# Kernel optimization log

Hardware: AMD Instinct MI355X
Metric: run time of the kernel (lower is better)

The kernel has to match this reference:

```python
import jax, jax.numpy as jnp
import numpy as np

N, D = 6144, 128
NUM_CLASSES, NUM_BATCHES = 20, 5
MIN_T, MAX_T = 0.1, 1.0
TEMP_BATCH = 0.5  # fixed per-batch-key temperature set in __init__
EPS = 1e-8        # F.cosine_similarity eps


def _class_weights(labels, n):
    c = jnp.bincount(labels, length=n).astype(jnp.float32)
    w = 1.0 / c
    return w / w.sum()


def setup_inputs() -> dict:
    key = jax.random.key(0)
    k1, k2, k3 = jax.random.split(key, 3)
    x = jax.random.normal(k1, (N, D), dtype=jnp.float32)
    targets = jax.random.randint(k2, (N,), 0, NUM_CLASSES)
    batch0 = jax.random.randint(k3, (N,), 0, NUM_BATCHES)
    return {
        "input": x,
        "temperature": jnp.float32(0.25),
        "weight_target": _class_weights(targets, NUM_CLASSES),
        "weight_batch0": _class_weights(batch0, NUM_BATCHES),
        "targets": targets,
        "batch0": batch0,
    }


def _snn_losses(S, pos_mask, neg_mask):
    # S: [N,N] exp-similarities; masks include/exclude self consistently with torch code
    diag = jnp.diagonal(S)
    pos_sum = jnp.einsum('ij,ij->i', S, pos_mask.astype(S.dtype)) - diag  # self is in pos_mask
    neg_sum = jnp.einsum('ij,ij->i', S, neg_mask.astype(S.dtype))
    cnt_pos = pos_mask.sum(axis=1)  # includes self
    cnt_neg = neg_mask.sum(axis=1)
    valid = (cnt_pos >= 2) & (cnt_neg >= 1)
    pos_safe = jnp.where(valid, pos_sum, 1.0)
    neg_safe = jnp.where(valid, neg_sum, 1.0)
    loss_i = -jnp.log(pos_safe / (pos_safe + neg_safe))
    return loss_i, valid


def _weighted_class_sum(loss_i, valid, labels, weights, num_segments):
    lsum = jax.ops.segment_sum(jnp.where(valid, loss_i, 0.0), labels, num_segments=num_segments)
    cnt = jax.ops.segment_sum(valid.astype(jnp.float32), labels, num_segments=num_segments)
    mean = lsum / jnp.maximum(cnt, 1.0)
    return jnp.sum(jnp.where(cnt > 0, mean * weights, 0.0))


def reference(input, temperature, weight_target, weight_batch0, targets, batch0):
    t = jnp.clip(temperature, MIN_T, MAX_T)
    norms = jnp.maximum(jnp.linalg.norm(input, axis=1, keepdims=True), EPS)
    xn = input / norms
    sim = xn @ xn.T  # [N, N] cosine similarity

    same_t = targets[:, None] == targets[None, :]

    # ----- target (cell-type) SNN loss -----
    S_t = jnp.exp(sim / t)
    loss_i, valid = _snn_losses(S_t, same_t, ~same_t)
    loss_target = _weighted_class_sum(loss_i, valid, targets, weight_target, NUM_CLASSES)

    # ----- batch-effect loss (one batch key), reciprocal of -log -----
    S_b = jnp.exp(sim / TEMP_BATCH)
    same_b = batch0[:, None] == batch0[None, :]
    pos_mask = same_t & same_b
    neg_mask = same_t & (~same_b)
    loss_bi, valid_b = _snn_losses(S_b, pos_mask, neg_mask)
    loss_bi = jnp.where(valid_b, 1.0 / jnp.where(valid_b, loss_bi, 1.0), 0.0)
    loss_batch = _weighted_class_sum(loss_bi, valid_b, batch0, weight_batch0, NUM_BATCHES)
    # single batch key -> mean over batch keys is just loss_batch

    return 0.9 * loss_target + 0.1 * loss_batch
```

## Files before the change

kernel.cpp:

```cpp
#include <hip/hip_runtime.h>
#include <hip/hip_bf16.h>
#include <math.h>

#define NN 6144
#define DD 128
#define NCLS 20
#define NBATCH 5
#define NB 48
#define NPAIR (NB * (NB + 1) / 2)

typedef float f32x4 __attribute__((ext_vector_type(4)));
typedef short bf16x8 __attribute__((ext_vector_type(8)));

#define SOFF (NN * DD / 2)
#define AOFF (SOFF + 4 * NN)
#define COFF (AOFF + 50)

__global__ __launch_bounds__(256) void k_prep(const float* __restrict__ x,
                                              float* __restrict__ ws) {
    const int t = threadIdx.x;
    if (blockIdx.x < 24) {
        float4 z = {0.f, 0.f, 0.f, 0.f};
        *(float4*)(ws + SOFF + blockIdx.x * 1024 + t * 4) = z;
    } else if (blockIdx.x == 24) {
        if (t < 51) ws[AOFF + t] = 0.0f;
    }
    const int lane = t & 63;
    const int row = blockIdx.x * 4 + (t >> 6);
    float2 v = *(const float2*)(x + row * DD + 2 * lane);
    float s = v.x * v.x + v.y * v.y;
#pragma unroll
    for (int m = 1; m < 64; m <<= 1) s += __shfl_xor(s, m, 64);
    float rinv = 1.0f / fmaxf(sqrtf(s), 1e-8f);
    __hip_bfloat16 h0 = __float2bfloat16(v.x * rinv);
    __hip_bfloat16 h1 = __float2bfloat16(v.y * rinv);
    ushort2 u;
    u.x = *(ushort*)&h0;
    u.y = *(ushort*)&h1;
    ushort* xnb = (ushort*)ws;
    *(ushort2*)(xnb + row * DD + 2 * lane) = u;
}

#define RED16(v)                                                      \
    {                                                                 \
        float s0 = up3 ? v[0] : v[2], k0 = up3 ? v[2] : v[0];         \
        float s1 = up3 ? v[1] : v[3], k1 = up3 ? v[3] : v[1];         \
        v[0] = k0 + __shfl_xor(s0, 8, 64);                            \
        v[1] = k1 + __shfl_xor(s1, 8, 64);                            \
        float s2 = up2 ? v[0] : v[1], k2 = up2 ? v[1] : v[0];         \
        v[0] = k2 + __shfl_xor(s2, 4, 64);                            \
        v[0] += __shfl_xor(v[0], 2, 64);                              \
        v[0] += __shfl_xor(v[0], 1, 64);                              \
    }

#define RED4(v)                                                       \
    {                                                                 \
        float s0 = q1 ? v[0] : v[2], k0 = q1 ? v[2] : v[0];           \
        float s1 = q1 ? v[1] : v[3], k1 = q1 ? v[3] : v[1];           \
        v[0] = k0 + __shfl_xor(s0, 32, 64);                           \
        v[1] = k1 + __shfl_xor(s1, 32, 64);                           \
        float s2 = q0 ? v[0] : v[1], k2 = q0 ? v[1] : v[0];           \
        v[0] = k2 + __shfl_xor(s2, 16, 64);                           \
    }

__global__ __launch_bounds__(256) void k_main(const float* __restrict__ temp,
                                              const int* __restrict__ tg,
                                              const int* __restrict__ bt,
                                              float* __restrict__ ws) {
    __shared__ ushort tA[128][72];
    __shared__ ushort tB[128][72];
    __shared__ int tgA[128], btA[128], tgB[128], btB[128];
    __shared__ float sRow[2][4][128];
    __shared__ float sCol[2][4][128];

    const ushort* xnb = (const ushort*)ws;
    float* PT = ws + SOFF;
    float* TT = PT + NN;
    float* PB = PT + 2 * NN;
    float* TB = PT + 3 * NN;

    int bi = 0, rem = blockIdx.x;
    while (rem >= NB - bi) { rem -= NB - bi; ++bi; }
    const int bj = bi + rem;
    const int I = bi * 128, J = bj * 128;
    const bool isDiag = (bi == bj);

    const int t = threadIdx.x;
    const int w = t >> 6;
    const int lane = t & 63;
    const int tx16 = lane & 15;
    const int quad = lane >> 4;
    const int rowBase = (w >> 1) * 64;
    const int colBase = (w & 1) * 64;

    const float tc = fminf(fmaxf(temp[0], 0.1f), 1.0f);
    const float c1 = 1.4426950408889634f / tc;
    const float c2 = 2.8853900817779268f;

    if (t < 128) { tgA[t] = tg[I + t]; btA[t] = bt[I + t]; }
    else { int u2 = t - 128; tgB[u2] = tg[J + u2]; btB[u2] = bt[J + u2]; }
    {
        float* zr = &sRow[0][0][0];
        float* zc = &sCol[0][0][0];
#pragma unroll
        for (int i = 0; i < 4; ++i) { zr[t + 256 * i] = 0.f; zc[t + 256 * i] = 0.f; }
    }

    f32x4 acc[4][4];
#pragma unroll
    for (int mt = 0; mt < 4; ++mt)
#pragma unroll
        for (int nt = 0; nt < 4; ++nt) acc[mt][nt] = (f32x4){0.f, 0.f, 0.f, 0.f};

    for (int kc = 0; kc < 2; ++kc) {
        if (kc) __syncthreads();
        {
            const int r0 = t >> 3, ch = t & 7;
            const ushort* gA = xnb + (I + r0) * DD + kc * 64 + ch * 8;
            const ushort* gB = xnb + (J + r0) * DD + kc * 64 + ch * 8;
#pragma unroll
            for (int it = 0; it < 4; ++it) {
                *(float4*)&tA[r0 + 32 * it][ch * 8] = *(const float4*)(gA + 32 * it * DD);
                *(float4*)&tB[r0 + 32 * it][ch * 8] = *(const float4*)(gB + 32 * it * DD);
            }
        }
        __syncthreads();
#pragma unroll
        for (int ks = 0; ks < 2; ++ks) {
            bf16x8 a[4], b[4];
            const int ko = ks * 32 + quad * 8;
#pragma unroll
            for (int mt = 0; mt < 4; ++mt)
                a[mt] = *(const bf16x8*)&tA[rowBase + 16 * mt + tx16][ko];
#pragma unroll
            for (int nt = 0; nt < 4; ++nt)
                b[nt] = *(const bf16x8*)&tB[colBase + 16 * nt + tx16][ko];
#pragma unroll
            for (int mt = 0; mt < 4; ++mt)
#pragma unroll
                for (int nt = 0; nt < 4; ++nt)
                    acc[mt][nt] = __builtin_amdgcn_mfma_f32_16x16x32_bf16(
                        a[mt], b[nt], acc[mt][nt], 0, 0, 0);
        }
    }

    float cPT[4] = {0}, cTT[4] = {0}, cPB[4] = {0}, cTB[4] = {0};
    int tjv[4], bjv[4];
#pragma unroll
    for (int nt = 0; nt < 4; ++nt) {
        int jl = colBase + 16 * nt + tx16;
        tjv[nt] = tgB[jl];
        bjv[nt] = btB[jl];
    }
    const bool up3 = (tx16 >> 3) & 1;
    const bool up2 = (tx16 >> 2) & 1;
    const int pOwn = tx16 >> 2;

#pragma unroll
    for (int mt = 0; mt < 4; ++mt) {
        float rPT[4] = {0}, rTT[4] = {0}, rPB[4] = {0}, rTB[4] = {0};
        int til[4], bil[4];
#pragma unroll
        for (int p = 0; p < 4; ++p) {
            int il = rowBase + 16 * mt + 4 * quad + p;
            til[p] = tgA[il];
            bil[p] = btA[il];
        }
#pragma unroll
        for (int nt = 0; nt < 4; ++nt) {
            const int jl = colBase + 16 * nt + tx16;
#pragma unroll
            for (int p = 0; p < 4; ++p) {
                const int il = rowBase + 16 * mt + 4 * quad + p;
                float s = acc[mt][nt][p];
                float et = __builtin_amdgcn_exp2f(c1 * s);
                float eb = __builtin_amdgcn_exp2f(c2 * s);
                bool nd = !isDiag || (il != jl);
                bool st = (til[p] == tjv[nt]) && nd;
                bool sb = (bil[p] == bjv[nt]);
                rTT[p] += nd ? et : 0.f;
                rPT[p] += st ? et : 0.f;
                rTB[p] += st ? eb : 0.f;
                rPB[p] += (st && sb) ? eb : 0.f;
                if (!isDiag) {
                    cTT[nt] += et;
                    cPT[nt] += st ? et : 0.f;
                    cTB[nt] += st ? eb : 0.f;
                    cPB[nt] += (st && sb) ? eb : 0.f;
                }
            }
        }
        RED16(rPT);
        RED16(rTT);
        RED16(rPB);
        RED16(rTB);
        if ((tx16 & 3) == 0) {
            int il = rowBase + 16 * mt + 4 * quad + pOwn;
            sRow[w & 1][0][il] = rPT[0];
            sRow[w & 1][1][il] = rTT[0];
            sRow[w & 1][2][il] = rPB[0];
            sRow[w & 1][3][il] = rTB[0];
        }
    }
    if (!isDiag) {
        const bool q1 = (quad >> 1) & 1;
        const bool q0 = quad & 1;
        RED4(cPT);
        RED4(cTT);
        RED4(cPB);
        RED4(cTB);
        int cl = colBase + 16 * quad + tx16;
        sCol[w >> 1][0][cl] = cPT[0];
        sCol[w >> 1][1][cl] = cTT[0];
        sCol[w >> 1][2][cl] = cPB[0];
        sCol[w >> 1][3][cl] = cTB[0];
    }

    __syncthreads();
    if (t < 128) {
        int gi = I + t;
        atomicAdd(&PT[gi], sRow[0][0][t] + sRow[1][0][t]);
        atomicAdd(&TT[gi], sRow[0][1][t] + sRow[1][1][t]);
        atomicAdd(&PB[gi], sRow[0][2][t] + sRow[1][2][t]);
        atomicAdd(&TB[gi], sRow[0][3][t] + sRow[1][3][t]);
    } else if (!isDiag) {
        int u2 = t - 128;
        int gj = J + u2;
        atomicAdd(&PT[gj], sCol[0][0][u2] + sCol[1][0][u2]);
        atomicAdd(&TT[gj], sCol[0][1][u2] + sCol[1][1][u2]);
        atomicAdd(&PB[gj], sCol[0][2][u2] + sCol[1][2][u2]);
        atomicAdd(&TB[gj], sCol[0][3][u2] + sCol[1][3][u2]);
    }
}

__global__ __launch_bounds__(256) void k_fin(const int* __restrict__ tg,
                                             const int* __restrict__ bt,
                                             const float* __restrict__ wt,
                                             const float* __restrict__ wb,
                                             float* __restrict__ ws,
                                             float* __restrict__ out) {
    __shared__ int hh[NCLS + NCLS * NBATCH];
    __shared__ float ph[4][52];
    __shared__ int lastFlag;
    const int t = threadIdx.x;
    const int wv = t >> 6;
    if (t < NCLS + NCLS * NBATCH) hh[t] = 0;
    if (t < 52 * 4) ((float*)ph)[t] = 0.0f;
    __syncthreads();
    for (int i = t; i < NN; i += 256) {
        int c = tg[i], b = bt[i];
        atomicAdd(&hh[c], 1);
        atomicAdd(&hh[NCLS + c * NBATCH + b], 1);
    }
    __syncthreads();
    const float* PT = ws + SOFF;
    const float* TT = PT + NN;
    const float* PB = PT + 2 * NN;
    const float* TB = PT + 3 * NN;
    {
        const int i = blockIdx.x * 256 + t;
        float pt = PT[i], tt = TT[i], pb = PB[i], tb = TB[i];
        int ti = tg[i], bi = bt[i];
        int cp = hh[ti];
        int cpb = hh[NCLS + ti * NBATCH + bi];
        if (cp >= 2 && (NN - cp) >= 1) {
            float loss = logf(tt) - logf(pt);
            atomicAdd(&ph[wv][ti], loss);
            atomicAdd(&ph[wv][20 + ti], 1.0f);
        }
        if (cpb >= 2 && (cp - cpb) >= 1) {
            float lb = logf(tb) - logf(pb);
            atomicAdd(&ph[wv][40 + bi], 1.0f / lb);
            atomicAdd(&ph[wv][45 + bi], 1.0f);
        }
    }
    __syncthreads();
    if (t < 50) {
        float s = ph[0][t] + ph[1][t] + ph[2][t] + ph[3][t];
        atomicAdd(&ws[AOFF + t], s);
    }
    __syncthreads();
    if (t == 0) {
        __threadfence();
        int old = atomicAdd((int*)(ws + COFF), 1);
        lastFlag = (old == 23) ? 1 : 0;
    }
    __syncthreads();
    if (lastFlag) {
        __threadfence();
        if (t < 64) {
            const float* acc = ws + AOFF;
            float term = 0.0f;
            if (t < NCLS) {
                float cnt = acc[NCLS + t];
                if (cnt > 0.f) term = 0.9f * (acc[t] / cnt) * wt[t];
            } else if (t >= 32 && t < 32 + NBATCH) {
                int b = t - 32;
                float cnt = acc[2 * NCLS + NBATCH + b];
                if (cnt > 0.f) term = 0.1f * (acc[2 * NCLS + b] / cnt) * wb[b];
            }
#pragma unroll
            for (int m = 1; m < 64; m <<= 1) term += __shfl_xor(term, m, 64);
            if (t == 0) out[0] = term;
        }
    }
}

extern "C" void kernel_launch(void* const* d_in, const int* in_sizes, int n_in,
                              void* d_out, int out_size, void* d_ws, size_t ws_size,
                              hipStream_t stream) {
    const float* x    = (const float*)d_in[0];
    const float* temp = (const float*)d_in[1];
    const float* wt   = (const float*)d_in[2];
    const float* wb   = (const float*)d_in[3];
    const int*   tg   = (const int*)d_in[4];
    const int*   bt   = (const int*)d_in[5];
    float* out = (float*)d_out;
    float* ws = (float*)d_ws;

    k_prep<<<NN / 4, 256, 0, stream>>>(x, ws);
    k_main<<<NPAIR, 256, 0, stream>>>(temp, tg, bt, ws);
    k_fin<<<24, 256, 0, stream>>>(tg, bt, wt, wb, ws, out);
}
```

Measured before the change: 102.6 us.

## Fuse finalize into main kernel via last-block reduction and alias shared memory

```diff
diff --git a/kernel.cpp b/kernel.cpp
--- a/kernel.cpp
+++ b/kernel.cpp
@@ -13,8 +13,7 @@
 typedef short bf16x8 __attribute__((ext_vector_type(8)));
 
 #define SOFF (NN * DD / 2)
-#define AOFF (SOFF + 4 * NN)
-#define COFF (AOFF + 50)
+#define COFF (SOFF + 4 * NN)
 
 __global__ __launch_bounds__(256) void k_prep(const float* __restrict__ x,
                                               float* __restrict__ ws) {
@@ -23,7 +22,7 @@
         float4 z = {0.f, 0.f, 0.f, 0.f};
         *(float4*)(ws + SOFF + blockIdx.x * 1024 + t * 4) = z;
     } else if (blockIdx.x == 24) {
-        if (t < 51) ws[AOFF + t] = 0.0f;
+        if (t == 0) ((int*)ws)[COFF] = 0;
     }
     const int lane = t & 63;
     const int row = blockIdx.x * 4 + (t >> 6);
@@ -66,12 +65,18 @@
 __global__ __launch_bounds__(256) void k_main(const float* __restrict__ temp,
                                               const int* __restrict__ tg,
                                               const int* __restrict__ bt,
-                                              float* __restrict__ ws) {
-    __shared__ ushort tA[128][72];
-    __shared__ ushort tB[128][72];
+                                              const float* __restrict__ wt,
+                                              const float* __restrict__ wb,
+                                              float* __restrict__ ws,
+                                              float* __restrict__ out) {
+    __shared__ __align__(16) char smem[34816];
     __shared__ int tgA[128], btA[128], tgB[128], btB[128];
-    __shared__ float sRow[2][4][128];
-    __shared__ float sCol[2][4][128];
+    __shared__ int lastFlag;
+
+    ushort (*tA)[68] = (ushort(*)[68])smem;
+    ushort (*tB)[68] = (ushort(*)[68])(smem + 17408);
+    float* sRowF = (float*)smem;
+    float* sColF = (float*)(smem + 4096);
 
     const ushort* xnb = (const ushort*)ws;
     float* PT = ws + SOFF;
@@ -99,12 +104,6 @@
 
     if (t < 128) { tgA[t] = tg[I + t]; btA[t] = bt[I + t]; }
     else { int u2 = t - 128; tgB[u2] = tg[J + u2]; btB[u2] = bt[J + u2]; }
-    {
-        float* zr = &sRow[0][0][0];
-        float* zc = &sCol[0][0][0];
-#pragma unroll
-        for (int i = 0; i < 4; ++i) { zr[t + 256 * i] = 0.f; zc[t + 256 * i] = 0.f; }
-    }
 
     f32x4 acc[4][4];
 #pragma unroll
@@ -144,6 +143,8 @@
         }
     }
 
+    __syncthreads();
+
     float cPT[4] = {0}, cTT[4] = {0}, cPB[4] = {0}, cTB[4] = {0};
     int tjv[4], bjv[4];
 #pragma unroll
@@ -166,27 +167,46 @@
             til[p] = tgA[il];
             bil[p] = btA[il];
         }
-#pragma unroll
-        for (int nt = 0; nt < 4; ++nt) {
-            const int jl = colBase + 16 * nt + tx16;
-#pragma unroll
-            for (int p = 0; p < 4; ++p) {
-                const int il = rowBase + 16 * mt + 4 * quad + p;
-                float s = acc[mt][nt][p];
-                float et = __builtin_amdgcn_exp2f(c1 * s);
-                float eb = __builtin_amdgcn_exp2f(c2 * s);
-                bool nd = !isDiag || (il != jl);
-                bool st = (til[p] == tjv[nt]) && nd;
-                bool sb = (bil[p] == bjv[nt]);
-                rTT[p] += nd ? et : 0.f;
-                rPT[p] += st ? et : 0.f;
-                rTB[p] += st ? eb : 0.f;
-                rPB[p] += (st && sb) ? eb : 0.f;
-                if (!isDiag) {
+        if (isDiag) {
+#pragma unroll
+            for (int nt = 0; nt < 4; ++nt) {
+                const int jl = colBase + 16 * nt + tx16;
+#pragma unroll
+                for (int p = 0; p < 4; ++p) {
+                    const int il = rowBase + 16 * mt + 4 * quad + p;
+                    float s = acc[mt][nt][p];
+                    float et = __builtin_amdgcn_exp2f(c1 * s);
+                    float eb = __builtin_amdgcn_exp2f(c2 * s);
+                    bool nd = (il != jl);
+                    bool st = (til[p] == tjv[nt]) && nd;
+                    bool sb = (bil[p] == bjv[nt]);
+                    rTT[p] += nd ? et : 0.f;
+                    rPT[p] += st ? et : 0.f;
+                    rTB[p] += st ? eb : 0.f;
+                    rPB[p] += (st && sb) ? eb : 0.f;
+                }
+            }
+        } else {
+#pragma unroll
+            for (int nt = 0; nt < 4; ++nt) {
+#pragma unroll
+                for (int p = 0; p < 4; ++p) {
+                    float s = acc[mt][nt][p];
+                    float et = __builtin_amdgcn_exp2f(c1 * s);
+                    float eb = __builtin_amdgcn_exp2f(c2 * s);
+                    bool st = (til[p] == tjv[nt]);
+                    bool sb = (bil[p] == bjv[nt]);
+                    float etp = st ? et : 0.f;
+                    float ebp = st ? eb : 0.f;
+                    float ebb = (st && sb) ? eb : 0.f;
+                    rTT[p] += et;
+                    rPT[p] += etp;
+                    rTB[p] += ebp;
+                    rPB[p] += ebb;
                     cTT[nt] += et;
-                    cPT[nt] += st ? et : 0.f;
-                    cTB[nt] += st ? eb : 0.f;
-                    cPB[nt] += (st && sb) ? eb : 0.f;
+                    cPT[nt] += etp;
+                    cTB[nt] += ebp;
+                    cPB[nt] += ebb;
                 }
             }
         }
@@ -196,10 +216,11 @@
         RED16(rTB);
         if ((tx16 & 3) == 0) {
             int il = rowBase + 16 * mt + 4 * quad + pOwn;
-            sRow[w & 1][0][il] = rPT[0];
-            sRow[w & 1][1][il] = rTT[0];
-            sRow[w & 1][2][il] = rPB[0];
-            sRow[w & 1][3][il] = rTB[0];
+            int rep = (w & 1) * 512;
+            sRowF[rep + 0 * 128 + il] = rPT[0];
+            sRowF[rep + 1 * 128 + il] = rTT[0];
+            sRowF[rep + 2 * 128 + il] = rPB[0];
+            sRowF[rep + 3 * 128 + il] = rTB[0];
         }
     }
     if (!isDiag) {
@@ -210,99 +231,87 @@
         RED4(cPB);
         RED4(cTB);
         int cl = colBase + 16 * quad + tx16;
-        sCol[w >> 1][0][cl] = cPT[0];
-        sCol[w >> 1][1][cl] = cTT[0];
-        sCol[w >> 1][2][cl] = cPB[0];
-        sCol[w >> 1][3][cl] = cTB[0];
+        int rep = (w >> 1) * 512;
+        sColF[rep + 0 * 128 + cl] = cPT[0];
+        sColF[rep + 1 * 128 + cl] = cTT[0];
+        sColF[rep + 2 * 128 + cl] = cPB[0];
+        sColF[rep + 3 * 128 + cl] = cTB[0];
     }
 
     __syncthreads();
     if (t < 128) {
         int gi = I + t;
-        atomicAdd(&PT[gi], sRow[0][0][t] + sRow[1][0][t]);
-        atomicAdd(&TT[gi], sRow[0][1][t] + sRow[1][1][t]);
-        atomicAdd(&PB[gi], sRow[0][2][t] + sRow[1][2][t]);
-        atomicAdd(&TB[gi], sRow[0][3][t] + sRow[1][3][t]);
+        atomicAdd(&PT[gi], sRowF[0 * 128 + t] + sRowF[512 + 0 * 128 + t]);
+        atomicAdd(&TT[gi], sRowF[1 * 128 + t] + sRowF[512 + 1 * 128 + t]);
+        atomicAdd(&PB[gi], sRowF[2 * 128 + t] + sRowF[512 + 2 * 128 + t]);
+        atomicAdd(&TB[gi], sRowF[3 * 128 + t] + sRowF[512 + 3 * 128 + t]);
     } else if (!isDiag) {
         int u2 = t - 128;
         int gj = J + u2;
-        atomicAdd(&PT[gj], sCol[0][0][u2] + sCol[1][0][u2]);
-        atomicAdd(&TT[gj], sCol[0][1][u2] + sCol[1][1][u2]);
-        atomicAdd(&PB[gj], sCol[0][2][u2] + sCol[1][2][u2]);
-        atomicAdd(&TB[gj], sCol[0][3][u2] + sCol[1][3][u2]);
-    }
-}
-
-__global__ __launch_bounds__(256) void k_fin(const int* __restrict__ tg,
-                                             const int* __restrict__ bt,
-                                             const float* __restrict__ wt,
-                                             const float* __restrict__ wb,
-                                             float* __restrict__ ws,
-                                             float* __restrict__ out) {
-    __shared__ int hh[NCLS + NCLS * NBATCH];
-    __shared__ float ph[4][52];
-    __shared__ int lastFlag;
-    const int t = threadIdx.x;
-    const int wv = t >> 6;
-    if (t < NCLS + NCLS * NBATCH) hh[t] = 0;
-    if (t < 52 * 4) ((float*)ph)[t] = 0.0f;
+        atomicAdd(&PT[gj], sColF[0 * 128 + u2] + sColF[512 + 0 * 128 + u2]);
+        atomicAdd(&TT[gj], sColF[1 * 128 + u2] + sColF[512 + 1 * 128 + u2]);
+        atomicAdd(&PB[gj], sColF[2 * 128 + u2] + sColF[512 + 2 * 128 + u2]);
+        atomicAdd(&TB[gj], sColF[3 * 128 + u2] + sColF[512 + 3 * 128 + u2]);
+    }
+
+    if (t == 0) {
+        __threadfence();
+        lastFlag = (atomicAdd((int*)ws + COFF, 1) == NPAIR - 1);
+    }
+    __syncthreads();
+    if (!lastFlag) return;
+    __threadfence();
+
+    int* hw = (int*)smem;
+    int* comb = (int*)(smem + 1920);
+    float* ph = (float*)(smem + 2432);
+    const int wv = w;
+    for (int i = t; i < 4 * 120; i += 256) hw[i] = 0;
+    for (int i = t; i < 4 * 52; i += 256) ph[i] = 0.f;
     __syncthreads();
     for (int i = t; i < NN; i += 256) {
         int c = tg[i], b = bt[i];
-        atomicAdd(&hh[c], 1);
-        atomicAdd(&hh[NCLS + c * NBATCH + b], 1);
-    }
-    __syncthreads();
-    const float* PT = ws + SOFF;
-    const float* TT = PT + NN;
-    const float* PB = PT + 2 * NN;
-    const float* TB = PT + 3 * NN;
-    {
-        const int i = blockIdx.x * 256 + t;
-        float pt = PT[i], tt = TT[i], pb = PB[i], tb = TB[i];
-        int ti = tg[i], bi = bt[i];
-        int cp = hh[ti];
-        int cpb = hh[NCLS + ti * NBATCH + bi];
+        atomicAdd(&hw[wv * 120 + c], 1);
+        atomicAdd(&hw[wv * 120 + 20 + c * NBATCH + b], 1);
+    }
+    __syncthreads();
+    if (t < 120) comb[t] = hw[t] + hw[120 + t] + hw[240 + t] + hw[360 + t];
+    __syncthreads();
+    for (int i = t; i < NN; i += 256) {
+        float pt = atomicAdd(&PT[i], 0.0f);
+        float tt = atomicAdd(&TT[i], 0.0f);
+        float pb = atomicAdd(&PB[i], 0.0f);
+        float tb = atomicAdd(&TB[i], 0.0f);
+        int ti = tg[i], bi_ = bt[i];
+        int cp = comb[ti];
+        int cpb = comb[20 + ti * NBATCH + bi_];
         if (cp >= 2 && (NN - cp) >= 1) {
-            float loss = logf(tt) - logf(pt);
-            atomicAdd(&ph[wv][ti], loss);
-            atomicAdd(&ph[wv][20 + ti], 1.0f);
+            float loss = logf(tt / pt);
+            atomicAdd(&ph[wv * 52 + ti], loss);
+            atomicAdd(&ph[wv * 52 + 20 + ti], 1.0f);
         }
         if (cpb >= 2 && (cp - cpb) >= 1) {
-            float lb = logf(tb) - logf(pb);
-            atomicAdd(&ph[wv][40 + bi], 1.0f / lb);
-            atomicAdd(&ph[wv][45 + bi], 1.0f);
-        }
-    }
-    __syncthreads();
-    if (t < 50) {
-        float s = ph[0][t] + ph[1][t] + ph[2][t] + ph[3][t];
-        atomicAdd(&ws[AOFF + t], s);
-    }
-    __syncthreads();
-    if (t == 0) {
-        __threadfence();
-        int old = atomicAdd((int*)(ws + COFF), 1);
-        lastFlag = (old == 23) ? 1 : 0;
-    }
-    __syncthreads();
-    if (lastFlag) {
-        __threadfence();
-        if (t < 64) {
-            const float* acc = ws + AOFF;
-            float term = 0.0f;
-            if (t < NCLS) {
-                float cnt = acc[NCLS + t];
-                if (cnt > 0.f) term = 0.9f * (acc[t] / cnt) * wt[t];
-            } else if (t >= 32 && t < 32 + NBATCH) {
-                int b = t - 32;
-                float cnt = acc[2 * NCLS + NBATCH + b];
-                if (cnt > 0.f) term = 0.1f * (acc[2 * NCLS + b] / cnt) * wb[b];
-            }
-#pragma unroll
-            for (int m = 1; m < 64; m <<= 1) term += __shfl_xor(term, m, 64);
-            if (t == 0) out[0] = term;
-        }
+            float lb = logf(tb / pb);
+            atomicAdd(&ph[wv * 52 + 40 + bi_], 1.0f / lb);
+            atomicAdd(&ph[wv * 52 + 45 + bi_], 1.0f);
+        }
+    }
+    __syncthreads();
+    if (t < 52) ph[t] = ph[t] + ph[52 + t] + ph[104 + t] + ph[156 + t];
+    __syncthreads();
+    if (t < 64) {
+        float term = 0.0f;
+        if (t < NCLS) {
+            float cnt = ph[20 + t];
+            if (cnt > 0.f) term = 0.9f * (ph[t] / cnt) * wt[t];
+        } else if (t >= 32 && t < 32 + NBATCH) {
+            int b = t - 32;
+            float cnt = ph[45 + b];
+            if (cnt > 0.f) term = 0.1f * (ph[40 + b] / cnt) * wb[b];
+        }
+#pragma unroll
+        for (int m = 1; m < 64; m <<= 1) term += __shfl_xor(term, m, 64);
+        if (t == 0) out[0] = term;
     }
 }
 
@@ -319,6 +328,5 @@
     float* ws = (float*)d_ws;
 
     k_prep<<<NN / 4, 256, 0, stream>>>(x, ws);
-    k_main<<<NPAIR, 256, 0, stream>>>(temp, tg, bt, ws);
-    k_fin<<<24, 256, 0, stream>>>(tg, bt, wt, wb, ws, out);
+    k_main<<<NPAIR, 256, 0, stream>>>(temp, tg, bt, wt, wb, ws, out);
 }
```

Result: slower. 159.7 us (+55.7%).
